# Kernel tuning notes

Hardware: AMD Instinct MI355X
Metric: run time of the kernel (lower is better)

Reference implementation:

```python
import jax, jax.numpy as jnp
import numpy as np

B, S, H, F, E, K = 2, 1024, 2048, 512, 64, 8
CAP_FACTOR = 1.25


def setup_inputs() -> dict:
    key = jax.random.key(0)
    ks = jax.random.split(key, 8)
    sc = 0.02
    return {
        "x": jax.random.normal(ks[0], (B, S, H), jnp.float32),
        "router_w": jax.random.normal(ks[1], (H, E), jnp.float32) * sc,
        "wg": jax.random.normal(ks[2], (E, H, F), jnp.float32) * sc,
        "wu": jax.random.normal(ks[3], (E, H, F), jnp.float32) * sc,
        "wd": jax.random.normal(ks[4], (E, F, H), jnp.float32) * sc,
        "sw_g": jax.random.normal(ks[5], (2, H, 2 * F), jnp.float32) * sc,
        "sw_u": jax.random.normal(ks[6], (2, H, 2 * F), jnp.float32) * sc,
        "sw_d": jax.random.normal(ks[7], (2, 2 * F, H), jnp.float32) * sc,
    }


def reference(x, router_w, wg, wu, wd, sw_g, sw_u, sw_d):
    b, s, h = x.shape
    e = router_w.shape[1]
    T = b * s
    C = int(T * K / e * CAP_FACTOR)  # per-expert capacity
    xf = x.reshape(T, h)

    # --- router: linear -> softmax -> top-K sparse weights ---
    logits = xf @ router_w                       # [T,E]
    probs = jax.nn.softmax(logits, axis=-1)
    topv, topi = jax.lax.top_k(probs, K)         # [T,K]

    # --- capacity-based dispatch (positions within each expert) ---
    oh = jax.nn.one_hot(topi, e, dtype=jnp.float32)      # [T,K,E]
    ohf = oh.transpose(1, 0, 2).reshape(K * T, e)        # assignment order: k-major
    pos = jnp.cumsum(ohf, axis=0) - ohf                  # count of prior assignments
    pos_own = jnp.sum(pos * ohf, axis=1).astype(jnp.int32)  # [K*T]
    keep = pos_own < C
    e_flat = topi.T.reshape(K * T)
    w_flat = topv.T.reshape(K * T) * keep                # dropped tokens get 0 weight
    t_flat = jnp.tile(jnp.arange(T), K)
    slot = jnp.where(keep, pos_own, C)                   # overflow -> dummy slot C

    xd = jnp.zeros((e, C + 1, h), x.dtype).at[e_flat, slot].set(xf[t_flat])  # [E,C+1,H]

    # --- grouped expert FFN: spike-gated MLP down(relu(x Wg) * (x Wu)) ---
    hg = jax.nn.relu(jnp.einsum('ech,ehf->ecf', xd, wg))
    hu = jnp.einsum('ech,ehf->ecf', xd, wu)
    y = jnp.einsum('ecf,efh->ech', hg * hu, wd)          # [E,C+1,H]

    # --- weighted combine (scatter-add back to tokens) ---
    contrib = y[e_flat, slot] * w_flat[:, None]
    expert_out = jnp.zeros_like(xf).at[t_flat].add(contrib)

    # --- shared experts (always active) ---
    hs = jax.nn.relu(jnp.einsum('th,ehf->tef', xf, sw_g)) * jnp.einsum('th,ehf->tef', xf, sw_u)
    shared_out = jnp.einsum('tef,efh->th', hs, sw_d)     # sums the 2 shared experts

    out = (shared_out + expert_out).reshape(b, s, h)

    # --- load-balance aux loss ---
    frac = jnp.mean(jnp.sum(oh, axis=1), axis=0) / K     # dispatch fraction per expert
    mean_prob = jnp.mean(probs, axis=0)
    aux_loss = e * jnp.sum(frac * mean_prob)
    return out, aux_loss
```

## Files before the change

### kernel.cpp

```cpp
#include <hip/hip_runtime.h>

#define T_TOK 2048
#define HDIM  2048
#define NEXP  64
#define FDIM  512
#define KSEL  8
#define CAP   320
#define F2    1024

typedef __attribute__((ext_vector_type(8))) short bf16x8;
typedef __attribute__((ext_vector_type(4))) float f32x4;

__device__ __forceinline__ unsigned int pkbf(float a, float b) {
  unsigned int ua = __builtin_bit_cast(unsigned int, a);
  unsigned int ub = __builtin_bit_cast(unsigned int, b);
  return ((ua + 0x8000u) >> 16) | ((ub + 0x8000u) & 0xFFFF0000u);
}
__device__ __forceinline__ unsigned short f2bf(float a) {
  unsigned int ua = __builtin_bit_cast(unsigned int, a);
  return (unsigned short)((ua + 0x8000u) >> 16);
}

__global__ void cvt_kernel(const float* __restrict__ x, unsigned short* __restrict__ xb) {
  int i = blockIdx.x * 256 + threadIdx.x;
  float4 v = reinterpret_cast<const float4*>(x)[i];
  uint2 o;
  o.x = pkbf(v.x, v.y);
  o.y = pkbf(v.z, v.w);
  reinterpret_cast<uint2*>(xb)[i] = o;
}

__global__ __launch_bounds__(256) void router_kernel(
    const float* __restrict__ x, const float* __restrict__ rw,
    int* __restrict__ topi, float* __restrict__ topv, float* __restrict__ probsum) {
  __shared__ float ps[64];
  int tid = threadIdx.x;
  int wv = tid >> 6, lane = tid & 63;
  if (tid < 64) ps[tid] = 0.f;
  __syncthreads();
  int t = blockIdx.x * 4 + wv;
  const float* xrow = x + (long)t * HDIM;
  const float* wcol = rw + lane;
  double acc = 0.0;
#pragma unroll 8
  for (int h = 0; h < HDIM; h++)
    acc += (double)xrow[h] * (double)wcol[h * 64];
  float logit = (float)acc;
  float mx = logit;
  for (int off = 32; off; off >>= 1) mx = fmaxf(mx, __shfl_xor(mx, off));
  float ex = expf(logit - mx);
  float sm = ex;
  for (int off = 32; off; off >>= 1) sm += __shfl_xor(sm, off);
  float prob = ex / sm;
  atomicAdd(&ps[lane], prob);
  float p = prob;
  for (int k = 0; k < 8; k++) {
    float bv = p; int bi = lane;
    for (int off = 32; off; off >>= 1) {
      float ov = __shfl_xor(bv, off); int oi = __shfl_xor(bi, off);
      if (ov > bv || (ov == bv && oi < bi)) { bv = ov; bi = oi; }
    }
    if (lane == k) { topv[t * 8 + k] = bv; topi[t * 8 + k] = bi; }
    if (lane == bi) p = -1.f;
  }
  __syncthreads();
  if (tid < 64) atomicAdd(&probsum[tid], ps[tid]);
}

__global__ void rank_kernel(const int* __restrict__ topi, int* __restrict__ lrank,
                            int* __restrict__ hist) {
  __shared__ int ear[256];
  __shared__ unsigned short lr[256];
  int b = blockIdx.x, tid = threadIdx.x;
  int i = b * 256 + tid;
  int t = i & (T_TOK - 1), k = i >> 11;
  ear[tid] = topi[t * 8 + k];
  __syncthreads();
  if (tid < 64) {
    int c = 0;
    for (int j = 0; j < 256; j++)
      if (ear[j] == tid) { lr[j] = (unsigned short)c; c++; }
    hist[b * 64 + tid] = c;
  }
  __syncthreads();
  lrank[i] = lr[tid];
}

__global__ void scan_kernel(const int* __restrict__ hist, int* __restrict__ basetab,
                            int* __restrict__ cnt, const float* __restrict__ probsum,
                            float* __restrict__ aux_out) {
  int e = threadIdx.x;
  int run = 0;
  for (int b = 0; b < 64; b++) { basetab[b * 64 + e] = run; run += hist[b * 64 + e]; }
  cnt[e] = run;
  float v = (float)run * probsum[e];
  for (int off = 32; off; off >>= 1) v += __shfl_xor(v, off);
  if (e == 0) aux_out[0] = 64.0f * v / ((float)(KSEL * T_TOK) * (float)T_TOK);
}

__global__ void build_kernel(const int* __restrict__ topi, const float* __restrict__ topv,
                             const int* __restrict__ lrank, const int* __restrict__ basetab,
                             int* __restrict__ idx_tab, float* __restrict__ wt_tab) {
  int b = blockIdx.x, tid = threadIdx.x;
  int i = b * 256 + tid;
  int t = i & (T_TOK - 1), k = i >> 11;
  int e = topi[t * 8 + k];
  int slot = basetab[b * 64 + e] + lrank[i];
  if (slot < CAP) {
    idx_tab[e * CAP + slot] = t;
    wt_tab[e * CAP + slot] = topv[t * 8 + k];
  }
}

template <int N, int KD, int LDA, bool GATHER, bool HASWT>
__global__ __launch_bounds__(256) void gemm_gate_up(
    const unsigned short* __restrict__ Ab, long aStride,
    const int* __restrict__ idx, int idxStride,
    const float* __restrict__ Bg_, const float* __restrict__ Bu_, long bStride,
    const float* __restrict__ wt_,
    unsigned short* __restrict__ H_, long hStride, int M) {
  __shared__ unsigned short As[128 * 40];
  __shared__ unsigned short Bgs[128 * 40];
  __shared__ unsigned short Bus[128 * 40];
  int z = blockIdx.z;
  const unsigned short* A = Ab + (long)z * aStride;
  const float* Bg = Bg_ + (long)z * bStride;
  const float* Bu = Bu_ + (long)z * bStride;
  const int* idxp = GATHER ? idx + (long)z * idxStride : nullptr;
  const float* wtp = HASWT ? wt_ + (long)z * idxStride : nullptr;
  unsigned short* Hout = H_ + (long)z * hStride;
  int mt = blockIdx.y, nt = blockIdx.x;
  int tid = threadIdx.x;

  int arow = tid >> 1;
  int aseg = (tid & 1) * 2;
  int arow_g = mt * 128 + arow;
  long asrc = -1;
  if (arow_g < M) {
    int s = GATHER ? idxp[arow_g] : arow_g;
    if (s >= 0) asrc = (long)s * LDA;
  }
  unsigned short* adst = &As[arow * 40 + aseg * 8];

  int nn = tid & 127;
  int kh = tid >> 7;
  const float* bgp = Bg + (long)(kh * 16) * N + (nt * 128 + nn);
  const float* bup = Bu + (long)(kh * 16) * N + (nt * 128 + nn);
  unsigned short* bgd = &Bgs[nn * 40 + kh * 16];
  unsigned short* bud = &Bus[nn * 40 + kh * 16];

  int lane = tid & 63, quad = lane >> 4, r = lane & 15;
  int wv = tid >> 6, wm = wv & 1, wn = wv >> 1;

  f32x4 accg[4][4] = {};
  f32x4 accu[4][4] = {};

  for (int k0 = 0; k0 < KD; k0 += 32) {
    uint4 a0 = {0, 0, 0, 0}, a1 = {0, 0, 0, 0};
    if (asrc >= 0) {
      const uint4* ap = reinterpret_cast<const uint4*>(A + asrc + k0 + aseg * 8);
      a0 = ap[0]; a1 = ap[1];
    }
    float tg[16], tu[16];
    const float* bg0 = bgp + (long)k0 * N;
    const float* bu0 = bup + (long)k0 * N;
#pragma unroll
    for (int j = 0; j < 16; j++) { tg[j] = bg0[j * N]; tu[j] = bu0[j * N]; }
    *reinterpret_cast<uint4*>(adst) = a0;
    *reinterpret_cast<uint4*>(adst + 8) = a1;
    uint4 g0, g1, u0, u1;
    g0.x = pkbf(tg[0], tg[1]);  g0.y = pkbf(tg[2], tg[3]);
    g0.z = pkbf(tg[4], tg[5]);  g0.w = pkbf(tg[6], tg[7]);
    g1.x = pkbf(tg[8], tg[9]);  g1.y = pkbf(tg[10], tg[11]);
    g1.z = pkbf(tg[12], tg[13]); g1.w = pkbf(tg[14], tg[15]);
    u0.x = pkbf(tu[0], tu[1]);  u0.y = pkbf(tu[2], tu[3]);
    u0.z = pkbf(tu[4], tu[5]);  u0.w = pkbf(tu[6], tu[7]);
    u1.x = pkbf(tu[8], tu[9]);  u1.y = pkbf(tu[10], tu[11]);
    u1.z = pkbf(tu[12], tu[13]); u1.w = pkbf(tu[14], tu[15]);
    *reinterpret_cast<uint4*>(bgd) = g0;
    *reinterpret_cast<uint4*>(bgd + 8) = g1;
    *reinterpret_cast<uint4*>(bud) = u0;
    *reinterpret_cast<uint4*>(bud + 8) = u1;
    __syncthreads();
    bf16x8 af[4], bgf[4], buf2[4];
#pragma unroll
    for (int bm = 0; bm < 4; bm++)
      af[bm] = *reinterpret_cast<const bf16x8*>(&As[(wm * 64 + bm * 16 + r) * 40 + quad * 8]);
#pragma unroll
    for (int bn = 0; bn < 4; bn++) {
      bgf[bn] = *reinterpret_cast<const bf16x8*>(&Bgs[(wn * 64 + bn * 16 + r) * 40 + quad * 8]);
      buf2[bn] = *reinterpret_cast<const bf16x8*>(&Bus[(wn * 64 + bn * 16 + r) * 40 + quad * 8]);
    }
#pragma unroll
    for (int bm = 0; bm < 4; bm++)
#pragma unroll
      for (int bn = 0; bn < 4; bn++) {
        accg[bm][bn] = __builtin_amdgcn_mfma_f32_16x16x32_bf16(af[bm], bgf[bn], accg[bm][bn], 0, 0, 0);
        accu[bm][bn] = __builtin_amdgcn_mfma_f32_16x16x32_bf16(af[bm], buf2[bn], accu[bm][bn], 0, 0, 0);
      }
    __syncthreads();
  }
#pragma unroll
  for (int bm = 0; bm < 4; bm++)
#pragma unroll
    for (int i = 0; i < 4; i++) {
      int m = mt * 128 + wm * 64 + bm * 16 + quad * 4 + i;
      if (m < M) {
        float w = HASWT ? wtp[m] : 1.0f;
#pragma unroll
        for (int bn = 0; bn < 4; bn++) {
          int n = nt * 128 + wn * 64 + bn * 16 + r;
          float g = accg[bm][bn][i];
          float u = accu[bm][bn][i];
          float h = (g > 0.f ? g : 0.f) * u * w;
          Hout[(long)m * N + n] = f2bf(h);
        }
      }
    }
}

template <int N, int KD, int LDA, bool SCATTER>
__global__ __launch_bounds__(256) void gemm_down(
    const unsigned short* __restrict__ Ab, long aStride,
    const float* __restrict__ B_, long bStride,
    const int* __restrict__ idx, int idxStride,
    float* __restrict__ out, int M) {
  __shared__ unsigned short As[128 * 40];
  __shared__ unsigned short Bs[128 * 40];
  int z = blockIdx.z;
  const unsigned short* A = Ab + (long)z * aStride;
  const float* B = B_ + (long)z * bStride;
  const int* idxp = SCATTER ? idx + (long)z * idxStride : nullptr;
  int mt = blockIdx.y, nt = blockIdx.x;
  int tid = threadIdx.x;

  int arow = tid >> 1;
  int aseg = (tid & 1) * 2;
  int arow_g = mt * 128 + arow;
  long asrc = (arow_g < M) ? (long)arow_g * LDA : -1;
  unsigned short* adst = &As[arow * 40 + aseg * 8];

  int nn = tid & 127;
  int kh = tid >> 7;
  const float* bp = B + (long)(kh * 16) * N + (nt * 128 + nn);
  unsigned short* bd = &Bs[nn * 40 + kh * 16];

  int lane = tid & 63, quad = lane >> 4, r = lane & 15;
  int wv = tid >> 6, wm = wv & 1, wn = wv >> 1;

  f32x4 acc[4][4] = {};

  for (int k0 = 0; k0 < KD; k0 += 32) {
    uint4 a0 = {0, 0, 0, 0}, a1 = {0, 0, 0, 0};
    if (asrc >= 0) {
      const uint4* ap = reinterpret_cast<const uint4*>(A + asrc + k0 + aseg * 8);
      a0 = ap[0]; a1 = ap[1];
    }
    float tb[16];
    const float* b0 = bp + (long)k0 * N;
#pragma unroll
    for (int j = 0; j < 16; j++) tb[j] = b0[j * N];
    *reinterpret_cast<uint4*>(adst) = a0;
    *reinterpret_cast<uint4*>(adst + 8) = a1;
    uint4 w0, w1;
    w0.x = pkbf(tb[0], tb[1]);  w0.y = pkbf(tb[2], tb[3]);
    w0.z = pkbf(tb[4], tb[5]);  w0.w = pkbf(tb[6], tb[7]);
    w1.x = pkbf(tb[8], tb[9]);  w1.y = pkbf(tb[10], tb[11]);
    w1.z = pkbf(tb[12], tb[13]); w1.w = pkbf(tb[14], tb[15]);
    *reinterpret_cast<uint4*>(bd) = w0;
    *reinterpret_cast<uint4*>(bd + 8) = w1;
    __syncthreads();
    bf16x8 af[4], bf[4];
#pragma unroll
    for (int bm = 0; bm < 4; bm++)
      af[bm] = *reinterpret_cast<const bf16x8*>(&As[(wm * 64 + bm * 16 + r) * 40 + quad * 8]);
#pragma unroll
    for (int bn = 0; bn < 4; bn++)
      bf[bn] = *reinterpret_cast<const bf16x8*>(&Bs[(wn * 64 + bn * 16 + r) * 40 + quad * 8]);
#pragma unroll
    for (int bm = 0; bm < 4; bm++)
#pragma unroll
      for (int bn = 0; bn < 4; bn++)
        acc[bm][bn] = __builtin_amdgcn_mfma_f32_16x16x32_bf16(af[bm], bf[bn], acc[bm][bn], 0, 0, 0);
    __syncthreads();
  }
#pragma unroll
  for (int bm = 0; bm < 4; bm++)
#pragma unroll
    for (int i = 0; i < 4; i++) {
      int m = mt * 128 + wm * 64 + bm * 16 + quad * 4 + i;
      if (m < M) {
        int tok = SCATTER ? idxp[m] : m;
        if (tok >= 0) {
          float* orow = out + (long)tok * HDIM;
#pragma unroll
          for (int bn = 0; bn < 4; bn++) {
            int n = nt * 128 + wn * 64 + bn * 16 + r;
            atomicAdd(orow + n, acc[bm][bn][i]);
          }
        }
      }
    }
}

extern "C" void kernel_launch(void* const* d_in, const int* in_sizes, int n_in,
                              void* d_out, int out_size, void* d_ws, size_t ws_size,
                              hipStream_t stream) {
  const float* x   = (const float*)d_in[0];
  const float* rw  = (const float*)d_in[1];
  const float* wg  = (const float*)d_in[2];
  const float* wu  = (const float*)d_in[3];
  const float* wd  = (const float*)d_in[4];
  const float* swg = (const float*)d_in[5];
  const float* swu = (const float*)d_in[6];
  const float* swd = (const float*)d_in[7];
  float* out = (float*)d_out;

  char* ws = (char*)d_ws;
  size_t off = 0;
  auto alloc = [&](size_t bytes) -> char* {
    char* p = ws + off;
    off = (off + bytes + 255) & ~(size_t)255;
    return p;
  };
  unsigned short* xbf   = (unsigned short*)alloc((size_t)T_TOK * HDIM * 2);
  unsigned short* hbuf  = (unsigned short*)alloc((size_t)NEXP * CAP * FDIM * 2);
  unsigned short* hsbuf = (unsigned short*)alloc((size_t)2 * T_TOK * F2 * 2);
  int*   topi    = (int*)alloc(T_TOK * KSEL * 4);
  float* topv    = (float*)alloc(T_TOK * KSEL * 4);
  int*   lrank   = (int*)alloc(T_TOK * KSEL * 4);
  int*   hist    = (int*)alloc(64 * 64 * 4);
  int*   basetab = (int*)alloc(64 * 64 * 4);
  int*   cnt     = (int*)alloc(64 * 4);
  float* probsum = (float*)alloc(64 * 4);
  int*   idx_tab = (int*)alloc(NEXP * CAP * 4);
  float* wt_tab  = (float*)alloc(NEXP * CAP * 4);

  hipMemsetAsync(out, 0, (size_t)T_TOK * HDIM * 4, stream);
  hipMemsetAsync(probsum, 0, 64 * 4, stream);
  hipMemsetAsync(idx_tab, 0xFF, NEXP * CAP * 4, stream);
  hipMemsetAsync(wt_tab, 0, NEXP * CAP * 4, stream);

  cvt_kernel<<<T_TOK * HDIM / 4 / 256, 256, 0, stream>>>(x, xbf);
  router_kernel<<<T_TOK / 4, 256, 0, stream>>>(x, rw, topi, topv, probsum);
  rank_kernel<<<64, 256, 0, stream>>>(topi, lrank, hist);
  scan_kernel<<<1, 64, 0, stream>>>(hist, basetab, cnt, probsum, out + (size_t)T_TOK * HDIM);
  build_kernel<<<64, 256, 0, stream>>>(topi, topv, lrank, basetab, idx_tab, wt_tab);

  gemm_gate_up<FDIM, HDIM, HDIM, true, true><<<dim3(FDIM / 128, (CAP + 127) / 128, NEXP), 256, 0, stream>>>(
      xbf, 0L, idx_tab, CAP, wg, wu, (long)HDIM * FDIM, wt_tab, hbuf, (long)CAP * FDIM, CAP);
  gemm_gate_up<F2, HDIM, HDIM, false, false><<<dim3(F2 / 128, T_TOK / 128, 2), 256, 0, stream>>>(
      xbf, 0L, nullptr, 0, swg, swu, (long)HDIM * F2, nullptr, hsbuf, (long)T_TOK * F2, T_TOK);
  gemm_down<HDIM, FDIM, FDIM, true><<<dim3(HDIM / 128, (CAP + 127) / 128, NEXP), 256, 0, stream>>>(
      hbuf, (long)CAP * FDIM, wd, (long)FDIM * HDIM, idx_tab, CAP, out, CAP);
  gemm_down<HDIM, F2, F2, false><<<dim3(HDIM / 128, T_TOK / 128, 2), 256, 0, stream>>>(
      hsbuf, (long)T_TOK * F2, swd, (long)F2 * HDIM, nullptr, 0, out, T_TOK);
}
```

Measured before the change: 1.345 ms.

## Double-buffer GEMM tiles with register prefetch, shrink M tile, fuse shared down GEMM

```diff
diff --git a/kernel.cpp b/kernel.cpp
--- a/kernel.cpp
+++ b/kernel.cpp
@@ -112,193 +112,213 @@
   }
 }
 
-template <int N, int KD, int LDA, bool GATHER, bool HASWT>
+
+struct RawGU { uint4 a; float2 g[8]; float2 u[8]; };
+struct RawD  { uint4 a; float2 b[8]; };
+
+template <int N, bool GATHER, bool HASWT>
 __global__ __launch_bounds__(256) void gemm_gate_up(
-    const unsigned short* __restrict__ Ab, long aStride,
+    const unsigned short* __restrict__ Ab,
     const int* __restrict__ idx, int idxStride,
     const float* __restrict__ Bg_, const float* __restrict__ Bu_, long bStride,
     const float* __restrict__ wt_,
-    unsigned short* __restrict__ H_, long hStride, int M) {
-  __shared__ unsigned short As[128 * 40];
-  __shared__ unsigned short Bgs[128 * 40];
-  __shared__ unsigned short Bus[128 * 40];
-  int z = blockIdx.z;
-  const unsigned short* A = Ab + (long)z * aStride;
-  const float* Bg = Bg_ + (long)z * bStride;
-  const float* Bu = Bu_ + (long)z * bStride;
+    unsigned short* __restrict__ H_, long hStride, int ldH) {
+  constexpr int SA = 34;
+  __shared__ unsigned short As[2][64 * SA];
+  __shared__ unsigned short Bgs[2][128 * SA];
+  __shared__ unsigned short Bus[2][128 * SA];
+  const int z = blockIdx.z;
+  const int mt = blockIdx.y, nt = blockIdx.x;
+  const int tid = threadIdx.x;
+  const float* Bg = Bg_ + (long)z * bStride + nt * 128;
+  const float* Bu = Bu_ + (long)z * bStride + nt * 128;
   const int* idxp = GATHER ? idx + (long)z * idxStride : nullptr;
   const float* wtp = HASWT ? wt_ + (long)z * idxStride : nullptr;
   unsigned short* Hout = H_ + (long)z * hStride;
-  int mt = blockIdx.y, nt = blockIdx.x;
-  int tid = threadIdx.x;
-
-  int arow = tid >> 1;
-  int aseg = (tid & 1) * 2;
-  int arow_g = mt * 128 + arow;
+
+  const int arow = tid >> 2, achk = tid & 3;
+  const int mg_a = mt * 64 + arow;
   long asrc = -1;
-  if (arow_g < M) {
-    int s = GATHER ? idxp[arow_g] : arow_g;
-    if (s >= 0) asrc = (long)s * LDA;
-  }
-  unsigned short* adst = &As[arow * 40 + aseg * 8];
-
-  int nn = tid & 127;
-  int kh = tid >> 7;
-  const float* bgp = Bg + (long)(kh * 16) * N + (nt * 128 + nn);
-  const float* bup = Bu + (long)(kh * 16) * N + (nt * 128 + nn);
-  unsigned short* bgd = &Bgs[nn * 40 + kh * 16];
-  unsigned short* bud = &Bus[nn * 40 + kh * 16];
-
-  int lane = tid & 63, quad = lane >> 4, r = lane & 15;
-  int wv = tid >> 6, wm = wv & 1, wn = wv >> 1;
-
-  f32x4 accg[4][4] = {};
-  f32x4 accu[4][4] = {};
-
-  for (int k0 = 0; k0 < KD; k0 += 32) {
-    uint4 a0 = {0, 0, 0, 0}, a1 = {0, 0, 0, 0};
-    if (asrc >= 0) {
-      const uint4* ap = reinterpret_cast<const uint4*>(A + asrc + k0 + aseg * 8);
-      a0 = ap[0]; a1 = ap[1];
-    }
-    float tg[16], tu[16];
-    const float* bg0 = bgp + (long)k0 * N;
-    const float* bu0 = bup + (long)k0 * N;
-#pragma unroll
-    for (int j = 0; j < 16; j++) { tg[j] = bg0[j * N]; tu[j] = bu0[j * N]; }
-    *reinterpret_cast<uint4*>(adst) = a0;
-    *reinterpret_cast<uint4*>(adst + 8) = a1;
-    uint4 g0, g1, u0, u1;
-    g0.x = pkbf(tg[0], tg[1]);  g0.y = pkbf(tg[2], tg[3]);
-    g0.z = pkbf(tg[4], tg[5]);  g0.w = pkbf(tg[6], tg[7]);
-    g1.x = pkbf(tg[8], tg[9]);  g1.y = pkbf(tg[10], tg[11]);
-    g1.z = pkbf(tg[12], tg[13]); g1.w = pkbf(tg[14], tg[15]);
-    u0.x = pkbf(tu[0], tu[1]);  u0.y = pkbf(tu[2], tu[3]);
-    u0.z = pkbf(tu[4], tu[5]);  u0.w = pkbf(tu[6], tu[7]);
-    u1.x = pkbf(tu[8], tu[9]);  u1.y = pkbf(tu[10], tu[11]);
-    u1.z = pkbf(tu[12], tu[13]); u1.w = pkbf(tu[14], tu[15]);
-    *reinterpret_cast<uint4*>(bgd) = g0;
-    *reinterpret_cast<uint4*>(bgd + 8) = g1;
-    *reinterpret_cast<uint4*>(bud) = u0;
-    *reinterpret_cast<uint4*>(bud + 8) = u1;
+  {
+    int s = GATHER ? idxp[mg_a] : mg_a;
+    if (s >= 0) asrc = (long)s * HDIM + achk * 8;
+  }
+  const int n2 = (tid & 63) * 2, kh = tid >> 6;
+  const float* bgp = Bg + (long)(kh * 8) * N + n2;
+  const float* bup = Bu + (long)(kh * 8) * N + n2;
+
+  const int lane = tid & 63, r = lane & 15, quad = lane >> 4;
+  const int wv = tid >> 6, wm = wv & 1, wn = wv >> 1;
+
+  f32x4 accg[2][4] = {}, accu[2][4] = {};
+  RawGU c0, c1;
+
+  auto loadT = [&](int k0, RawGU& rg) {
+    uint4 a = {0, 0, 0, 0};
+    if (asrc >= 0) a = *reinterpret_cast<const uint4*>(Ab + asrc + k0);
+    rg.a = a;
+    const float* pg = bgp + (long)k0 * N;
+    const float* pu = bup + (long)k0 * N;
+#pragma unroll
+    for (int j = 0; j < 8; j++) {
+      rg.g[j] = *reinterpret_cast<const float2*>(pg + (long)j * N);
+      rg.u[j] = *reinterpret_cast<const float2*>(pu + (long)j * N);
+    }
+  };
+  auto storeT = [&](const RawGU& rg, int buf) {
+    *reinterpret_cast<uint4*>(&As[buf][arow * SA + achk * 8]) = rg.a;
+    uint4 w;
+    w.x = pkbf(rg.g[0].x, rg.g[1].x); w.y = pkbf(rg.g[2].x, rg.g[3].x);
+    w.z = pkbf(rg.g[4].x, rg.g[5].x); w.w = pkbf(rg.g[6].x, rg.g[7].x);
+    *reinterpret_cast<uint4*>(&Bgs[buf][n2 * SA + kh * 8]) = w;
+    w.x = pkbf(rg.g[0].y, rg.g[1].y); w.y = pkbf(rg.g[2].y, rg.g[3].y);
+    w.z = pkbf(rg.g[4].y, rg.g[5].y); w.w = pkbf(rg.g[6].y, rg.g[7].y);
+    *reinterpret_cast<uint4*>(&Bgs[buf][(n2 + 1) * SA + kh * 8]) = w;
+    w.x = pkbf(rg.u[0].x, rg.u[1].x); w.y = pkbf(rg.u[2].x, rg.u[3].x);
+    w.z = pkbf(rg.u[4].x, rg.u[5].x); w.w = pkbf(rg.u[6].x, rg.u[7].x);
+    *reinterpret_cast<uint4*>(&Bus[buf][n2 * SA + kh * 8]) = w;
+    w.x = pkbf(rg.u[0].y, rg.u[1].y); w.y = pkbf(rg.u[2].y, rg.u[3].y);
+    w.z = pkbf(rg.u[4].y, rg.u[5].y); w.w = pkbf(rg.u[6].y, rg.u[7].y);
+    *reinterpret_cast<uint4*>(&Bus[buf][(n2 + 1) * SA + kh * 8]) = w;
+  };
+  auto compT = [&](int buf) {
+    bf16x8 a0 = *reinterpret_cast<const bf16x8*>(&As[buf][(wm * 32 + r) * SA + quad * 8]);
+    bf16x8 a1 = *reinterpret_cast<const bf16x8*>(&As[buf][(wm * 32 + 16 + r) * SA + quad * 8]);
+#pragma unroll
+    for (int bn = 0; bn < 4; bn++) {
+      bf16x8 b = *reinterpret_cast<const bf16x8*>(&Bgs[buf][(wn * 64 + bn * 16 + r) * SA + quad * 8]);
+      accg[0][bn] = __builtin_amdgcn_mfma_f32_16x16x32_bf16(a0, b, accg[0][bn], 0, 0, 0);
+      accg[1][bn] = __builtin_amdgcn_mfma_f32_16x16x32_bf16(a1, b, accg[1][bn], 0, 0, 0);
+    }
+#pragma unroll
+    for (int bn = 0; bn < 4; bn++) {
+      bf16x8 b = *reinterpret_cast<const bf16x8*>(&Bus[buf][(wn * 64 + bn * 16 + r) * SA + quad * 8]);
+      accu[0][bn] = __builtin_amdgcn_mfma_f32_16x16x32_bf16(a0, b, accu[0][bn], 0, 0, 0);
+      accu[1][bn] = __builtin_amdgcn_mfma_f32_16x16x32_bf16(a1, b, accu[1][bn], 0, 0, 0);
+    }
+  };
+
+  loadT(0, c0);
+  storeT(c0, 0);
+  loadT(32, c0);
+  __syncthreads();
+  constexpr int NK = HDIM / 32;
+#pragma unroll 1
+  for (int kt = 0; kt < NK; kt += 2) {
+    if (kt + 2 < NK) loadT((kt + 2) * 32, c1);
+    compT(0);
+    storeT(c0, 1);
     __syncthreads();
-    bf16x8 af[4], bgf[4], buf2[4];
-#pragma unroll
-    for (int bm = 0; bm < 4; bm++)
-      af[bm] = *reinterpret_cast<const bf16x8*>(&As[(wm * 64 + bm * 16 + r) * 40 + quad * 8]);
-#pragma unroll
-    for (int bn = 0; bn < 4; bn++) {
-      bgf[bn] = *reinterpret_cast<const bf16x8*>(&Bgs[(wn * 64 + bn * 16 + r) * 40 + quad * 8]);
-      buf2[bn] = *reinterpret_cast<const bf16x8*>(&Bus[(wn * 64 + bn * 16 + r) * 40 + quad * 8]);
-    }
-#pragma unroll
-    for (int bm = 0; bm < 4; bm++)
+    if (kt + 3 < NK) loadT((kt + 3) * 32, c0);
+    compT(1);
+    if (kt + 2 < NK) storeT(c1, 0);
+    __syncthreads();
+  }
+
+#pragma unroll
+  for (int bm = 0; bm < 2; bm++)
+#pragma unroll
+    for (int i = 0; i < 4; i++) {
+      int mg = mt * 64 + wm * 32 + bm * 16 + quad * 4 + i;
+      float w = HASWT ? wtp[mg] : 1.0f;
 #pragma unroll
       for (int bn = 0; bn < 4; bn++) {
-        accg[bm][bn] = __builtin_amdgcn_mfma_f32_16x16x32_bf16(af[bm], bgf[bn], accg[bm][bn], 0, 0, 0);
-        accu[bm][bn] = __builtin_amdgcn_mfma_f32_16x16x32_bf16(af[bm], buf2[bn], accu[bm][bn], 0, 0, 0);
+        int n = nt * 128 + wn * 64 + bn * 16 + r;
+        float g = accg[bm][bn][i], u = accu[bm][bn][i];
+        Hout[(long)mg * ldH + n] = f2bf(fmaxf(g, 0.f) * u * w);
       }
-    __syncthreads();
-  }
-#pragma unroll
-  for (int bm = 0; bm < 4; bm++)
-#pragma unroll
-    for (int i = 0; i < 4; i++) {
-      int m = mt * 128 + wm * 64 + bm * 16 + quad * 4 + i;
-      if (m < M) {
-        float w = HASWT ? wtp[m] : 1.0f;
-#pragma unroll
-        for (int bn = 0; bn < 4; bn++) {
-          int n = nt * 128 + wn * 64 + bn * 16 + r;
-          float g = accg[bm][bn][i];
-          float u = accu[bm][bn][i];
-          float h = (g > 0.f ? g : 0.f) * u * w;
-          Hout[(long)m * N + n] = f2bf(h);
-        }
-      }
-    }
-}
-
-template <int N, int KD, int LDA, bool SCATTER>
+    }
+}
+
+template <int KD, int LDA, bool SCATTER>
 __global__ __launch_bounds__(256) void gemm_down(
     const unsigned short* __restrict__ Ab, long aStride,
     const float* __restrict__ B_, long bStride,
     const int* __restrict__ idx, int idxStride,
-    float* __restrict__ out, int M) {
-  __shared__ unsigned short As[128 * 40];
-  __shared__ unsigned short Bs[128 * 40];
-  int z = blockIdx.z;
+    float* __restrict__ out) {
+  constexpr int SA = 34;
+  constexpr int N = HDIM;
+  __shared__ unsigned short As[2][64 * SA];
+  __shared__ unsigned short Bs[2][128 * SA];
+  const int z = blockIdx.z;
+  const int mt = blockIdx.y, nt = blockIdx.x;
+  const int tid = threadIdx.x;
   const unsigned short* A = Ab + (long)z * aStride;
-  const float* B = B_ + (long)z * bStride;
+  const float* B = B_ + (long)z * bStride + nt * 128;
   const int* idxp = SCATTER ? idx + (long)z * idxStride : nullptr;
-  int mt = blockIdx.y, nt = blockIdx.x;
-  int tid = threadIdx.x;
-
-  int arow = tid >> 1;
-  int aseg = (tid & 1) * 2;
-  int arow_g = mt * 128 + arow;
-  long asrc = (arow_g < M) ? (long)arow_g * LDA : -1;
-  unsigned short* adst = &As[arow * 40 + aseg * 8];
-
-  int nn = tid & 127;
-  int kh = tid >> 7;
-  const float* bp = B + (long)(kh * 16) * N + (nt * 128 + nn);
-  unsigned short* bd = &Bs[nn * 40 + kh * 16];
-
-  int lane = tid & 63, quad = lane >> 4, r = lane & 15;
-  int wv = tid >> 6, wm = wv & 1, wn = wv >> 1;
-
-  f32x4 acc[4][4] = {};
-
-  for (int k0 = 0; k0 < KD; k0 += 32) {
-    uint4 a0 = {0, 0, 0, 0}, a1 = {0, 0, 0, 0};
-    if (asrc >= 0) {
-      const uint4* ap = reinterpret_cast<const uint4*>(A + asrc + k0 + aseg * 8);
-      a0 = ap[0]; a1 = ap[1];
-    }
-    float tb[16];
-    const float* b0 = bp + (long)k0 * N;
-#pragma unroll
-    for (int j = 0; j < 16; j++) tb[j] = b0[j * N];
-    *reinterpret_cast<uint4*>(adst) = a0;
-    *reinterpret_cast<uint4*>(adst + 8) = a1;
-    uint4 w0, w1;
-    w0.x = pkbf(tb[0], tb[1]);  w0.y = pkbf(tb[2], tb[3]);
-    w0.z = pkbf(tb[4], tb[5]);  w0.w = pkbf(tb[6], tb[7]);
-    w1.x = pkbf(tb[8], tb[9]);  w1.y = pkbf(tb[10], tb[11]);
-    w1.z = pkbf(tb[12], tb[13]); w1.w = pkbf(tb[14], tb[15]);
-    *reinterpret_cast<uint4*>(bd) = w0;
-    *reinterpret_cast<uint4*>(bd + 8) = w1;
+
+  const int arow = tid >> 2, achk = tid & 3;
+  const long asrc = (long)(mt * 64 + arow) * LDA + achk * 8;
+  const int n2 = (tid & 63) * 2, kh = tid >> 6;
+  const float* bp = B + (long)(kh * 8) * N + n2;
+
+  const int lane = tid & 63, r = lane & 15, quad = lane >> 4;
+  const int wv = tid >> 6, wm = wv & 1, wn = wv >> 1;
+
+  f32x4 acc[2][4] = {};
+  RawD c0, c1;
+
+  auto loadT = [&](int k0, RawD& rg) {
+    rg.a = *reinterpret_cast<const uint4*>(A + asrc + k0);
+    const float* p = bp + (long)k0 * N;
+#pragma unroll
+    for (int j = 0; j < 8; j++)
+      rg.b[j] = *reinterpret_cast<const float2*>(p + (long)j * N);
+  };
+  auto storeT = [&](const RawD& rg, int buf) {
+    *reinterpret_cast<uint4*>(&As[buf][arow * SA + achk * 8]) = rg.a;
+    uint4 w;
+    w.x = pkbf(rg.b[0].x, rg.b[1].x); w.y = pkbf(rg.b[2].x, rg.b[3].x);
+    w.z = pkbf(rg.b[4].x, rg.b[5].x); w.w = pkbf(rg.b[6].x, rg.b[7].x);
+    *reinterpret_cast<uint4*>(&Bs[buf][n2 * SA + kh * 8]) = w;
+    w.x = pkbf(rg.b[0].y, rg.b[1].y); w.y = pkbf(rg.b[2].y, rg.b[3].y);
+    w.z = pkbf(rg.b[4].y, rg.b[5].y); w.w = pkbf(rg.b[6].y, rg.b[7].y);
+    *reinterpret_cast<uint4*>(&Bs[buf][(n2 + 1) * SA + kh * 8]) = w;
+  };
+  auto compT = [&](int buf) {
+    bf16x8 a0 = *reinterpret_cast<const bf16x8*>(&As[buf][(wm * 32 + r) * SA + quad * 8]);
+    bf16x8 a1 = *reinterpret_cast<const bf16x8*>(&As[buf][(wm * 32 + 16 + r) * SA + quad * 8]);
+#pragma unroll
+    for (int bn = 0; bn < 4; bn++) {
+      bf16x8 b = *reinterpret_cast<const bf16x8*>(&Bs[buf][(wn * 64 + bn * 16 + r) * SA + quad * 8]);
+      acc[0][bn] = __builtin_amdgcn_mfma_f32_16x16x32_bf16(a0, b, acc[0][bn], 0, 0, 0);
+      acc[1][bn] = __builtin_amdgcn_mfma_f32_16x16x32_bf16(a1, b, acc[1][bn], 0, 0, 0);
+    }
+  };
+
+  loadT(0, c0);
+  storeT(c0, 0);
+  loadT(32, c0);
+  __syncthreads();
+  constexpr int NK = KD / 32;
+#pragma unroll 1
+  for (int kt = 0; kt < NK; kt += 2) {
+    if (kt + 2 < NK) loadT((kt + 2) * 32, c1);
+    compT(0);
+    storeT(c0, 1);
     __syncthreads();
-    bf16x8 af[4], bf[4];
-#pragma unroll
-    for (int bm = 0; bm < 4; bm++)
-      af[bm] = *reinterpret_cast<const bf16x8*>(&As[(wm * 64 + bm * 16 + r) * 40 + quad * 8]);
-#pragma unroll
-    for (int bn = 0; bn < 4; bn++)
-      bf[bn] = *reinterpret_cast<const bf16x8*>(&Bs[(wn * 64 + bn * 16 + r) * 40 + quad * 8]);
-#pragma unroll
-    for (int bm = 0; bm < 4; bm++)
-#pragma unroll
-      for (int bn = 0; bn < 4; bn++)
-        acc[bm][bn] = __builtin_amdgcn_mfma_f32_16x16x32_bf16(af[bm], bf[bn], acc[bm][bn], 0, 0, 0);
+    if (kt + 3 < NK) loadT((kt + 3) * 32, c0);
+    compT(1);
+    if (kt + 2 < NK) storeT(c1, 0);
     __syncthreads();
   }
-#pragma unroll
-  for (int bm = 0; bm < 4; bm++)
+
+#pragma unroll
+  for (int bm = 0; bm < 2; bm++)
 #pragma unroll
     for (int i = 0; i < 4; i++) {
-      int m = mt * 128 + wm * 64 + bm * 16 + quad * 4 + i;
-      if (m < M) {
-        int tok = SCATTER ? idxp[m] : m;
+      int mg = mt * 64 + wm * 32 + bm * 16 + quad * 4 + i;
+      if (SCATTER) {
+        int tok = idxp[mg];
         if (tok >= 0) {
-          float* orow = out + (long)tok * HDIM;
-#pragma unroll
-          for (int bn = 0; bn < 4; bn++) {
-            int n = nt * 128 + wn * 64 + bn * 16 + r;
-            atomicAdd(orow + n, acc[bm][bn][i]);
-          }
+          float* orow = out + (long)tok * HDIM + nt * 128 + wn * 64 + r;
+#pragma unroll
+          for (int bn = 0; bn < 4; bn++) atomicAdd(orow + bn * 16, acc[bm][bn][i]);
         }
+      } else {
+        float* orow = out + (long)mg * HDIM + nt * 128 + wn * 64 + r;
+#pragma unroll
+        for (int bn = 0; bn < 4; bn++) orow[bn * 16] += acc[bm][bn][i];
       }
     }
 }
@@ -325,7 +345,7 @@
   };
   unsigned short* xbf   = (unsigned short*)alloc((size_t)T_TOK * HDIM * 2);
   unsigned short* hbuf  = (unsigned short*)alloc((size_t)NEXP * CAP * FDIM * 2);
-  unsigned short* hsbuf = (unsigned short*)alloc((size_t)2 * T_TOK * F2 * 2);
+  unsigned short* hsbuf = (unsigned short*)alloc((size_t)T_TOK * 2 * F2 * 2);
   int*   topi    = (int*)alloc(T_TOK * KSEL * 4);
   float* topv    = (float*)alloc(T_TOK * KSEL * 4);
   int*   lrank   = (int*)alloc(T_TOK * KSEL * 4);
@@ -347,12 +367,12 @@
   scan_kernel<<<1, 64, 0, stream>>>(hist, basetab, cnt, probsum, out + (size_t)T_TOK * HDIM);
   build_kernel<<<64, 256, 0, stream>>>(topi, topv, lrank, basetab, idx_tab, wt_tab);
 
-  gemm_gate_up<FDIM, HDIM, HDIM, true, true><<<dim3(FDIM / 128, (CAP + 127) / 128, NEXP), 256, 0, stream>>>(
-      xbf, 0L, idx_tab, CAP, wg, wu, (long)HDIM * FDIM, wt_tab, hbuf, (long)CAP * FDIM, CAP);
-  gemm_gate_up<F2, HDIM, HDIM, false, false><<<dim3(F2 / 128, T_TOK / 128, 2), 256, 0, stream>>>(
-      xbf, 0L, nullptr, 0, swg, swu, (long)HDIM * F2, nullptr, hsbuf, (long)T_TOK * F2, T_TOK);
-  gemm_down<HDIM, FDIM, FDIM, true><<<dim3(HDIM / 128, (CAP + 127) / 128, NEXP), 256, 0, stream>>>(
-      hbuf, (long)CAP * FDIM, wd, (long)FDIM * HDIM, idx_tab, CAP, out, CAP);
-  gemm_down<HDIM, F2, F2, false><<<dim3(HDIM / 128, T_TOK / 128, 2), 256, 0, stream>>>(
-      hsbuf, (long)T_TOK * F2, swd, (long)F2 * HDIM, nullptr, 0, out, T_TOK);
-}
+  gemm_gate_up<FDIM, true, true><<<dim3(FDIM / 128, CAP / 64, NEXP), 256, 0, stream>>>(
+      xbf, idx_tab, CAP, wg, wu, (long)HDIM * FDIM, wt_tab, hbuf, (long)CAP * FDIM, FDIM);
+  gemm_gate_up<F2, false, false><<<dim3(F2 / 128, T_TOK / 64, 2), 256, 0, stream>>>(
+      xbf, nullptr, 0, swg, swu, (long)HDIM * F2, nullptr, hsbuf, (long)F2, 2 * F2);
+  gemm_down<FDIM, FDIM, true><<<dim3(HDIM / 128, CAP / 64, NEXP), 256, 0, stream>>>(
+      hbuf, (long)CAP * FDIM, wd, (long)FDIM * HDIM, idx_tab, CAP, out);
+  gemm_down<2 * F2, 2 * F2, false><<<dim3(HDIM / 128, T_TOK / 64, 1), 256, 0, stream>>>(
+      hsbuf, 0L, swd, 0L, nullptr, 0, out);
+}
```

Result: no change. 1.337 ms (-0.6%).
